# Performance work log

Measured on AMD Instinct MI355X. Metric: run time of the kernel, lower is better.

The kernel has to match this reference:

```python
import jax, jax.numpy as jnp
import numpy as np

B, C_IN, H, W = 4, 256, 48, 48
HEADS, HD = 8, 64
N = H * W
SCALE = 1.0 / (HD ** 0.5)


def setup_inputs() -> dict:
    key = jax.random.key(0)
    ks = jax.random.split(key, 5)
    x = jax.random.normal(ks[0], (B, C_IN, H, W), dtype=jnp.float32)
    # 1x1 conv weights, squeezed: [heads, head_channels, in_channels]
    Wq = jax.random.normal(ks[1], (HEADS, HD, C_IN), dtype=jnp.float32) * (C_IN ** -0.5)
    Wk = jax.random.normal(ks[2], (HEADS, HD, C_IN), dtype=jnp.float32) * (C_IN ** -0.5)
    Wv = jax.random.normal(ks[3], (HEADS, HD, C_IN), dtype=jnp.float32) * (C_IN ** -0.5)
    # output 1x1 conv: [in_channels, heads*head_channels]
    Wo = jax.random.normal(ks[4], (C_IN, HEADS * HD), dtype=jnp.float32) * ((HEADS * HD) ** -0.5)
    return {"x": x, "Wq": Wq, "Wk": Wk, "Wv": Wv, "Wo": Wo}


def reference(x, Wq, Wk, Wv, Wo):
    b, c, h, w = x.shape
    n = h * w
    xf = x.reshape(b, c, n)  # [B, C, N]
    # per-head 1x1 convs == batched projections -> [heads, B, N, HD]
    q = jnp.einsum('hdc,bcn->hbnd', Wq, xf)
    k = jnp.einsum('hdc,bcn->hbnd', Wk, xf)
    v = jnp.einsum('hdc,bcn->hbnd', Wv, xf)
    scores = jnp.einsum('hbnd,hbmd->hbnm', q, k) * SCALE  # [heads, B, N, N]
    probs = jax.nn.softmax(scores, axis=-1)
    ws = jnp.einsum('hbnm,hbmd->hbnd', probs, v)  # [heads, B, N, HD]
    # faithful replication of torch: transpose(1,2) then reshape(B, heads*HD, H, W)
    ws = jnp.transpose(ws, (0, 2, 1, 3))  # [heads, N, B, HD]
    ws = ws.reshape(b, HEADS * HD, h, w)
    out = jnp.einsum('oc,bchw->bohw', Wo, ws)  # output 1x1 conv
    return out
```

## Files before the change

kernel.cpp:

```cpp
#include <hip/hip_runtime.h>

#define B_     4
#define CIN    256
#define NTOK   2304
#define HEADS  8
#define HD     64
#define SCALE  0.125f
#define LOG2E  1.44269504088896f
#define QSCALE (SCALE * LOG2E)
#define PBIAS  4.0f
#define QKV_ELEMS (HEADS * B_ * NTOK * HD)
#define HBSTRIDE 147456
#define WSZ    131072

typedef _Float16 f16;
typedef _Float16 __attribute__((ext_vector_type(8))) h8v;
typedef _Float16 __attribute__((ext_vector_type(4))) h4v;
typedef ushort   __attribute__((ext_vector_type(8))) us8;
typedef float    __attribute__((ext_vector_type(16))) f16v;

__device__ inline uint pk2(float a, float b) {
    auto v = __builtin_amdgcn_cvt_pkrtz(a, b);
    return __builtin_bit_cast(uint, v);
}
#define EXP2(x) __builtin_amdgcn_exp2f(x)

#define GLOAD_LDS(g, l) __builtin_amdgcn_global_load_lds( \
    (const __attribute__((address_space(1))) unsigned int*)(g), \
    (__attribute__((address_space(3))) unsigned int*)(l), 16, 0, 0)

__global__ __launch_bounds__(256) void prep(
    const float* __restrict__ x,
    const float* __restrict__ Wq, const float* __restrict__ Wk,
    const float* __restrict__ Wv, const float* __restrict__ Wo,
    f16* __restrict__ wc, f16* __restrict__ woc, f16* __restrict__ xt)
{
    __shared__ float T[64][65];
    const int bid = blockIdx.x;
    const int tid = threadIdx.x;

    if (bid < 512) {
        int e4 = (bid * 256 + tid) * 4;
        const float* src; f16* dst; float mult = 1.0f; int off;
        if (e4 < WSZ)          { src = Wq; off = e4;           dst = wc;           mult = QSCALE; }
        else if (e4 < 2 * WSZ) { src = Wk; off = e4 - WSZ;     dst = wc + WSZ; }
        else if (e4 < 3 * WSZ) { src = Wv; off = e4 - 2 * WSZ; dst = wc + 2 * WSZ; }
        else                   { src = Wo; off = e4 - 3 * WSZ; dst = woc; }
        float4 r = *(const float4*)(src + off);
        h4v hv;
        hv.x = (f16)(r.x * mult); hv.y = (f16)(r.y * mult);
        hv.z = (f16)(r.z * mult); hv.w = (f16)(r.w * mult);
        *(h4v*)(dst + off) = hv;
        return;
    }

    const int r  = bid - 512;
    const int n0 = (r % 36) * 64;
    const int c0 = ((r / 36) % 4) * 64;
    const int b  = r / 144;
    const float* sb = x + ((size_t)b * CIN + c0) * NTOK;
    #pragma unroll
    for (int i = 0; i < 16; ++i) {
        int idx = tid + 256 * i;
        int rr = idx >> 6, ll = idx & 63;
        T[ll][rr] = sb[(size_t)rr * NTOK + n0 + ll];
    }
    __syncthreads();
    const size_t ob = ((size_t)b * NTOK + n0) * CIN + c0;
    #pragma unroll
    for (int i = 0; i < 4; ++i) {
        int idx = tid + 256 * i;
        int row = idx >> 4, c4 = (idx & 15) * 4;
        h4v v;
        v.x = (f16)T[row][c4 + 0]; v.y = (f16)T[row][c4 + 1];
        v.z = (f16)T[row][c4 + 2]; v.w = (f16)T[row][c4 + 3];
        *(h4v*)(xt + ob + (size_t)row * CIN + c4) = v;
    }
}

__global__ __launch_bounds__(128) void proj_mfma(
    const f16* __restrict__ wc, const f16* __restrict__ xt,
    f16* __restrict__ qh, f16* __restrict__ kh, f16* __restrict__ vth)
{
    const int ntile = blockIdx.x;
    const int hp    = blockIdx.y;
    const int b     = blockIdx.z;
    const int p     = hp >> 3, h = hp & 7;
    const int hb    = h * 4 + b;
    const f16* Wp = wc + ((size_t)p * 8 + h) * (HD * CIN);

    __shared__ __align__(16) f16 Ws[2][64][64], Xs[2][64][64];

    const int tid = threadIdx.x;
    const int w = tid >> 6, lane = tid & 63;
    const int lm = lane & 31, lh = lane >> 5;
    const int n_loc  = w * 32 + lm;
    const int n_glob = ntile * 64 + n_loc;

    const f16* xb = xt + ((size_t)b * NTOK + ntile * 64) * CIN;

    auto stage = [&](int buf, int c0) {
        const f16* src = (w == 0) ? Wp : xb;
        f16* dst = (w == 0) ? &Ws[buf][0][0] : &Xs[buf][0][0];
        #pragma unroll
        for (int i = 0; i < 8; ++i) {
            int g = i * 64 + lane; int row = g >> 3; int c = (g & 7) ^ (row & 7);
            GLOAD_LDS(src + (size_t)row * CIN + c0 + c * 8, dst + i * 512);
        }
    };

    f16v o0, o1;
    #pragma unroll
    for (int i = 0; i < 16; ++i) { o0[i] = 0.f; o1[i] = 0.f; }

    stage(0, 0);
    for (int c0 = 0; c0 < CIN; c0 += 64) {
        const int cur = (c0 >> 6) & 1;
        __syncthreads();
        if (c0 + 64 < CIN) stage(cur ^ 1, c0 + 64);
        #pragma unroll
        for (int s = 0; s < 4; ++s) {
            const int pp = ((2 * s + lh) ^ (lm & 7)) * 8;
            h8v a0 = *(const h8v*)&Ws[cur][lm][pp];
            h8v a1 = *(const h8v*)&Ws[cur][lm + 32][pp];
            h8v bh = *(const h8v*)&Xs[cur][n_loc][pp];
            o0 = __builtin_amdgcn_mfma_f32_32x32x16_f16(a0, bh, o0, 0, 0, 0);
            o1 = __builtin_amdgcn_mfma_f32_32x32x16_f16(a1, bh, o1, 0, 0, 0);
        }
    }

    const size_t hboff = (size_t)hb * HBSTRIDE;
    if (p < 2) {
        f16* oh = ((p == 0) ? qh : kh) + hboff + (size_t)n_glob * 64;
        #pragma unroll
        for (int t = 0; t < 2; ++t) {
            const f16v& oc = t ? o1 : o0;
            #pragma unroll
            for (int g = 0; g < 4; ++g) {
                int d0 = 8 * g + 4 * lh + 32 * t;
                h4v hv;
                hv.x = (f16)oc[4 * g + 0]; hv.y = (f16)oc[4 * g + 1];
                hv.z = (f16)oc[4 * g + 2]; hv.w = (f16)oc[4 * g + 3];
                *(h4v*)(oh + d0) = hv;
            }
        }
    } else {
        f16* oh = vth + hboff;
        #pragma unroll
        for (int t = 0; t < 2; ++t) {
            const f16v& oc = t ? o1 : o0;
            #pragma unroll
            for (int r = 0; r < 16; ++r) {
                int d = (r & 3) + 8 * (r >> 2) + 4 * lh + 32 * t;
                oh[(size_t)d * NTOK + n_glob] = (f16)oc[r];
            }
        }
    }
}

__global__ __launch_bounds__(256, 1) void attn_mfma(
    const f16* __restrict__ qh, const f16* __restrict__ kh,
    const f16* __restrict__ vth, f16* __restrict__ wsth)
{
    const int bid   = blockIdx.x;
    const int xcd   = bid & 7;
    const int slot  = bid >> 3;
    const int hb    = xcd * 4 + (slot / 18);
    const int rpair = slot % 18;
    const int h_    = hb >> 2, b = hb & 3;
    const int tid   = threadIdx.x;
    const int w     = tid >> 6;
    const int lane  = tid & 63;
    const int lm    = lane & 31;
    const int lh    = lane >> 5;
    const int qg    = w >> 1;
    const int ks    = w & 1;

    __shared__ __align__(16) f16 SMEM[2][2][2][64][64];

    const size_t hboff = (size_t)hb * HBSTRIDE;
    const int mA = rpair * 128 + qg * 64 + lm;
    const int mB = mA + 32;

    h8v QfA[4], QfB[4];
    #pragma unroll
    for (int s = 0; s < 4; ++s) {
        QfA[s] = *(const h8v*)(qh + hboff + (size_t)mA * 64 + (2 * s + lh) * 8);
        QfB[s] = *(const h8v*)(qh + hboff + (size_t)mB * 64 + (2 * s + lh) * 8);
    }

    f16v oA0, oA1, oB0, oB1;
    f16v sA0, sA1, sB0, sB1;
    #pragma unroll
    for (int i = 0; i < 16; ++i) { oA0[i] = 0.f; oA1[i] = 0.f; oB0[i] = 0.f; oB1[i] = 0.f; }
    float lsumA = 0.f, lsumB = 0.f;
    h8v pfA[4], pfB[4];

    const int  sv  = w >> 1;
    const int  stp = w & 1;
    const f16* gb  = (sv == 0) ? kh + hboff : vth + hboff;

    auto stage = [&](int tb, int ti) {
        const int kts = 2 * ti + stp;
        f16* dst = &SMEM[sv][tb][stp][0][0];
        #pragma unroll
        for (int i = 0; i < 8; ++i) {
            int g   = i * 64 + lane;
            int row = g >> 3;
            int c   = (g & 7) ^ (row & 7);
            const f16* src = (sv == 0)
                ? gb + kts * 4096 + row * 64 + c * 8
                : gb + (size_t)row * 2304 + kts * 64 + c * 8;
            GLOAD_LDS(src, dst + i * 512);
        }
    };

    auto DO_QK = [&](int tb) {
        #pragma unroll
        for (int i = 0; i < 16; ++i) {
            sA0[i] = -PBIAS; sA1[i] = -PBIAS; sB0[i] = -PBIAS; sB1[i] = -PBIAS;
        }
        #pragma unroll
        for (int s = 0; s < 4; ++s) {
            const int p = ((2 * s + lh) ^ (lm & 7)) * 8;
            h8v k0 = *(const h8v*)&SMEM[0][tb][ks][lm][p];
            h8v k1 = *(const h8v*)&SMEM[0][tb][ks][lm + 32][p];
            sA0 = __builtin_amdgcn_mfma_f32_32x32x16_f16(k0, QfA[s], sA0, 0, 0, 0);
            sA1 = __builtin_amdgcn_mfma_f32_32x32x16_f16(k1, QfA[s], sA1, 0, 0, 0);
            sB0 = __builtin_amdgcn_mfma_f32_32x32x16_f16(k0, QfB[s], sB0, 0, 0, 0);
            sB1 = __builtin_amdgcn_mfma_f32_32x32x16_f16(k1, QfB[s], sB1, 0, 0, 0);
        }
    };

    auto DO_SM = [&]() {
        float pa0 = 0.f, pa1 = 0.f, pa2 = 0.f, pa3 = 0.f;
        float pb0 = 0.f, pb1 = 0.f, pb2 = 0.f, pb3 = 0.f;
        #pragma unroll
        for (int i = 0; i < 16; i += 4) {
            sA0[i+0] = EXP2(sA0[i+0]); pa0 += sA0[i+0];
            sA0[i+1] = EXP2(sA0[i+1]); pa1 += sA0[i+1];
            sA0[i+2] = EXP2(sA0[i+2]); pa2 += sA0[i+2];
            sA0[i+3] = EXP2(sA0[i+3]); pa3 += sA0[i+3];
        }
        #pragma unroll
        for (int i = 0; i < 16; i += 4) {
            sA1[i+0] = EXP2(sA1[i+0]); pa0 += sA1[i+0];
            sA1[i+1] = EXP2(sA1[i+1]); pa1 += sA1[i+1];
            sA1[i+2] = EXP2(sA1[i+2]); pa2 += sA1[i+2];
            sA1[i+3] = EXP2(sA1[i+3]); pa3 += sA1[i+3];
        }
        #pragma unroll
        for (int i = 0; i < 16; i += 4) {
            sB0[i+0] = EXP2(sB0[i+0]); pb0 += sB0[i+0];
            sB0[i+1] = EXP2(sB0[i+1]); pb1 += sB0[i+1];
            sB0[i+2] = EXP2(sB0[i+2]); pb2 += sB0[i+2];
            sB0[i+3] = EXP2(sB0[i+3]); pb3 += sB0[i+3];
        }
        #pragma unroll
        for (int i = 0; i < 16; i += 4) {
            sB1[i+0] = EXP2(sB1[i+0]); pb0 += sB1[i+0];
            sB1[i+1] = EXP2(sB1[i+1]); pb1 += sB1[i+1];
            sB1[i+2] = EXP2(sB1[i+2]); pb2 += sB1[i+2];
            sB1[i+3] = EXP2(sB1[i+3]); pb3 += sB1[i+3];
        }
        lsumA += (pa0 + pa1) + (pa2 + pa3);
        lsumB += (pb0 + pb1) + (pb2 + pb3);

        #pragma unroll
        for (int s = 0; s < 4; ++s) {
            const int q2 = 8 * (s & 1);
            const f16v& ja = (s >> 1) ? sA1 : sA0;
            const f16v& jb = (s >> 1) ? sB1 : sB0;
            uint a0 = pk2(ja[q2 + 0], ja[q2 + 1]);
            uint a1 = pk2(ja[q2 + 2], ja[q2 + 3]);
            uint a2 = pk2(ja[q2 + 4], ja[q2 + 5]);
            uint a3 = pk2(ja[q2 + 6], ja[q2 + 7]);
            auto a02 = __builtin_amdgcn_permlane32_swap(a0, a2, false, false);
            auto a13 = __builtin_amdgcn_permlane32_swap(a1, a3, false, false);
            uint4 ua = { a02[0], a13[0], a02[1], a13[1] };
            pfA[s] = __builtin_bit_cast(h8v, ua);
            uint b0 = pk2(jb[q2 + 0], jb[q2 + 1]);
            uint b1 = pk2(jb[q2 + 2], jb[q2 + 3]);
            uint b2 = pk2(jb[q2 + 4], jb[q2 + 5]);
            uint b3 = pk2(jb[q2 + 6], jb[q2 + 7]);
            auto b02 = __builtin_amdgcn_permlane32_swap(b0, b2, false, false);
            auto b13 = __builtin_amdgcn_permlane32_swap(b1, b3, false, false);
            uint4 ub = { b02[0], b13[0], b02[1], b13[1] };
            pfB[s] = __builtin_bit_cast(h8v, ub);
        }
    };

    auto DO_PV = [&](int tb) {
        #pragma unroll
        for (int s = 0; s < 4; ++s) {
            const int p = ((2 * s + lh) ^ (lm & 7)) * 8;
            h8v v0 = *(const h8v*)&SMEM[1][tb][ks][lm][p];
            h8v v1 = *(const h8v*)&SMEM[1][tb][ks][lm + 32][p];
            oA0 = __builtin_amdgcn_mfma_f32_32x32x16_f16(v0, pfA[s], oA0, 0, 0, 0);
            oA1 = __builtin_amdgcn_mfma_f32_32x32x16_f16(v1, pfA[s], oA1, 0, 0, 0);
            oB0 = __builtin_amdgcn_mfma_f32_32x32x16_f16(v0, pfB[s], oB0, 0, 0, 0);
            oB1 = __builtin_amdgcn_mfma_f32_32x32x16_f16(v1, pfB[s], oB1, 0, 0, 0);
        }
    };

    if (sv == 0) stage(0, 0);
    __syncthreads();

    stage(sv == 0 ? 1 : 0, sv == 0 ? 1 : 0);
    __builtin_amdgcn_s_setprio(1);
    DO_QK(0);
    __builtin_amdgcn_s_setprio(0);
    __syncthreads();

    for (int t = 1; t < 18; ++t) {
        if (sv == 0) { if (t < 17) stage((t + 1) & 1, t + 1); }
        else         stage(t & 1, t);

        DO_SM();
        __builtin_amdgcn_s_setprio(1);
        DO_PV((t - 1) & 1);
        DO_QK(t & 1);
        __builtin_amdgcn_s_setprio(0);
        __syncthreads();
    }

    DO_SM();
    __builtin_amdgcn_s_setprio(1);
    DO_PV(1);
    __builtin_amdgcn_s_setprio(0);
    __syncthreads();

    float* red = (float*)&SMEM[0][0][0][0][0];
    if (ks == 1) {
        float* dA = red + (size_t)(qg * 128 + lane) * 33;
        float* dB = red + (size_t)(qg * 128 + 64 + lane) * 33;
        #pragma unroll
        for (int i = 0; i < 16; ++i) {
            dA[i] = oA0[i]; dA[16 + i] = oA1[i];
            dB[i] = oB0[i]; dB[16 + i] = oB1[i];
        }
        dA[32] = lsumA; dB[32] = lsumB;
    }
    __syncthreads();
    if (ks == 0) {
        const float* sA = red + (size_t)(qg * 128 + lane) * 33;
        const float* sB = red + (size_t)(qg * 128 + 64 + lane) * 33;
        #pragma unroll
        for (int i = 0; i < 16; ++i) {
            oA0[i] += sA[i]; oA1[i] += sA[16 + i];
            oB0[i] += sB[i]; oB1[i] += sB[16 + i];
        }
        lsumA += sA[32]; lsumB += sB[32];
        lsumA += __shfl_xor(lsumA, 32);
        lsumB += __shfl_xor(lsumB, 32);
        float invA = 1.0f / lsumA, invB = 1.0f / lsumB;

        f16* wrA = wsth + ((size_t)h_ * NTOK + mA) * 256 + b * 64;
        f16* wrB = wsth + ((size_t)h_ * NTOK + mB) * 256 + b * 64;
        #pragma unroll
        for (int g = 0; g < 4; ++g) {
            h4v r0, r1;
            r0.x = (f16)(oA0[4 * g + 0] * invA); r0.y = (f16)(oA0[4 * g + 1] * invA);
            r0.z = (f16)(oA0[4 * g + 2] * invA); r0.w = (f16)(oA0[4 * g + 3] * invA);
            *(h4v*)(wrA + 8 * g + 4 * lh) = r0;
            r1.x = (f16)(oA1[4 * g + 0] * invA); r1.y = (f16)(oA1[4 * g + 1] * invA);
            r1.z = (f16)(oA1[4 * g + 2] * invA); r1.w = (f16)(oA1[4 * g + 3] * invA);
            *(h4v*)(wrA + 32 + 8 * g + 4 * lh) = r1;
        }
        #pragma unroll
        for (int g = 0; g < 4; ++g) {
            h4v r0, r1;
            r0.x = (f16)(oB0[4 * g + 0] * invB); r0.y = (f16)(oB0[4 * g + 1] * invB);
            r0.z = (f16)(oB0[4 * g + 2] * invB); r0.w = (f16)(oB0[4 * g + 3] * invB);
            *(h4v*)(wrB + 8 * g + 4 * lh) = r0;
            r1.x = (f16)(oB1[4 * g + 0] * invB); r1.y = (f16)(oB1[4 * g + 1] * invB);
            r1.z = (f16)(oB1[4 * g + 2] * invB); r1.w = (f16)(oB1[4 * g + 3] * invB);
            *(h4v*)(wrB + 32 + 8 * g + 4 * lh) = r1;
        }
    }
}

__global__ __launch_bounds__(128) void outconv_mfma(
    const f16* __restrict__ woc, const f16* __restrict__ ws,
    float* __restrict__ out)
{
    const int ntile = blockIdx.x;
    const int otile = blockIdx.y;
    const int b     = blockIdx.z;

    __shared__ __align__(16) f16 Wos[2][64][64];
    __shared__ __align__(16) f16 Xs[2][64][72];

    const int tid = threadIdx.x;
    const int w = tid >> 6, lane = tid & 63;
    const int lm = lane & 31, lh = lane >> 5;
    const int n_loc  = w * 32 + lm;
    const int n_glob = ntile * 64 + n_loc;
    const int pr = tid >> 2;
    const int qn = tid & 3;

    const f16* Wb = woc + (size_t)(otile * 64) * 512;
    const f16* wsb = ws + (size_t)b * 512 * NTOK + ntile * 64 + qn * 16;

    auto stageW = [&](int buf, int c0) {
        #pragma unroll
        for (int j = 0; j < 4; ++j) {
            int i = w * 4 + j;
            int g = i * 64 + lane; int row = g >> 3; int c = (g & 7) ^ (row & 7);
            GLOAD_LDS(Wb + (size_t)row * 512 + c0 + c * 8,
                      &Wos[buf][0][0] + i * 512);
        }
    };

    uint4 x0, x1, x2, x3;
    auto loadB = [&](int c0) {
        const f16* r0 = wsb + (size_t)(c0 + 2 * pr) * NTOK;
        const f16* r1 = r0 + NTOK;
        x0 = *(const uint4*)(r0);
        x1 = *(const uint4*)(r0 + 8);
        x2 = *(const uint4*)(r1);
        x3 = *(const uint4*)(r1 + 8);
    };
    auto storeB = [&](int buf) {
        us8 a0 = __builtin_bit_cast(us8, x0), a1 = __builtin_bit_cast(us8, x1);
        us8 b0 = __builtin_bit_cast(us8, x2), b1 = __builtin_bit_cast(us8, x3);
        #pragma unroll
        for (int j = 0; j < 8; ++j) {
            *(uint*)&Xs[buf][qn * 16 + j][2 * pr]     = (uint)a0[j] | ((uint)b0[j] << 16);
            *(uint*)&Xs[buf][qn * 16 + 8 + j][2 * pr] = (uint)a1[j] | ((uint)b1[j] << 16);
        }
    };

    f16v o0, o1;
    #pragma unroll
    for (int i = 0; i < 16; ++i) { o0[i] = 0.f; o1[i] = 0.f; }

    stageW(0, 0);
    loadB(0);
    storeB(0);
    for (int c0 = 0; c0 < 512; c0 += 64) {
        const int cur = (c0 >> 6) & 1;
        __syncthreads();
        if (c0 + 64 < 512) { stageW(cur ^ 1, c0 + 64); loadB(c0 + 64); }
        #pragma unroll
        for (int s = 0; s < 4; ++s) {
            const int pp = ((2 * s + lh) ^ (lm & 7)) * 8;
            const int co = (2 * s + lh) * 8;
            h8v a0 = *(const h8v*)&Wos[cur][lm][pp];
            h8v a1 = *(const h8v*)&Wos[cur][lm + 32][pp];
            h8v bh = *(const h8v*)&Xs[cur][n_loc][co];
            o0 = __builtin_amdgcn_mfma_f32_32x32x16_f16(a0, bh, o0, 0, 0, 0);
            o1 = __builtin_amdgcn_mfma_f32_32x32x16_f16(a1, bh, o1, 0, 0, 0);
        }
        if (c0 + 64 < 512) storeB(cur ^ 1);
    }

    #pragma unroll
    for (int t = 0; t < 2; ++t) {
        const f16v& oc = t ? o1 : o0;
        #pragma unroll
        for (int r = 0; r < 16; ++r) {
            int orow = otile * 64 + (r & 3) + 8 * (r >> 2) + 4 * lh + 32 * t;
            out[((size_t)b * CIN + orow) * NTOK + n_glob] = oc[r];
        }
    }
}

extern "C" void kernel_launch(void* const* d_in, const int* in_sizes, int n_in,
                              void* d_out, int out_size, void* d_ws, size_t ws_size,
                              hipStream_t stream)
{
    const float* x  = (const float*)d_in[0];
    const float* Wq = (const float*)d_in[1];
    const float* Wk = (const float*)d_in[2];
    const float* Wv = (const float*)d_in[3];
    const float* Wo = (const float*)d_in[4];
    float* out = (float*)d_out;

    f16* qh   = (f16*)d_ws;
    f16* kh   = qh   + QKV_ELEMS;
    f16* vth  = kh   + QKV_ELEMS;
    f16* wsth = vth  + QKV_ELEMS;
    f16* xt   = wsth;
    f16* wc   = wsth + QKV_ELEMS;
    f16* woc  = wc   + 3 * WSZ;

    prep<<<dim3(1088), 256, 0, stream>>>(x, Wq, Wk, Wv, Wo, wc, woc, xt);
    proj_mfma<<<dim3(36, 24, 4), 128, 0, stream>>>(wc, xt, qh, kh, vth);
    attn_mfma<<<dim3(576), 256, 0, stream>>>(qh, kh, vth, wsth);
    outconv_mfma<<<dim3(36, 4, 4), 128, 0, stream>>>(woc, wsth, out);
}
```

Baseline: 193.6 us.

## Shrink attention blocks to two waves with per-wave self-staged K/V

The attention kernel moves from 256-thread blocks (two query groups with a key-split pair each) to 128-thread blocks covering 64 queries, launched as 1152 blocks with launch_bounds allowing three blocks per CU. Each wave now stages its own K and V tiles into a private LDS slice and synchronises with explicit vmcnt/lgkmcnt waits in place of block-wide __syncthreads in the main loop. The aim is to raise occupancy so waves overlap loads with MFMA work, and to drop barrier costs. In exchange it loses the double-buffered K/V prefetch and reads Q once per smaller tile. The hand-placed waitcnt counts must match the number of outstanding loads, or the kernel can read stale LDS data.

```diff
diff --git a/kernel.cpp b/kernel.cpp
--- a/kernel.cpp
+++ b/kernel.cpp
@@ -28,6 +28,11 @@
 #define GLOAD_LDS(g, l) __builtin_amdgcn_global_load_lds( \
     (const __attribute__((address_space(1))) unsigned int*)(g), \
     (__attribute__((address_space(3))) unsigned int*)(l), 16, 0, 0)
+
+#define VMFENCE(N) do { asm volatile("s_waitcnt vmcnt(" #N ")" ::: "memory"); \
+                        __builtin_amdgcn_sched_barrier(0); } while (0)
+#define LGKFENCE() do { asm volatile("s_waitcnt lgkmcnt(0)" ::: "memory"); \
+                        __builtin_amdgcn_sched_barrier(0); } while (0)
 
 __global__ __launch_bounds__(256) void prep(
     const float* __restrict__ x,
@@ -158,28 +163,26 @@
     }
 }
 
-__global__ __launch_bounds__(256, 1) void attn_mfma(
+__global__ __launch_bounds__(128, 3) void attn_mfma(
     const f16* __restrict__ qh, const f16* __restrict__ kh,
     const f16* __restrict__ vth, f16* __restrict__ wsth)
 {
     const int bid   = blockIdx.x;
     const int xcd   = bid & 7;
     const int slot  = bid >> 3;
-    const int hb    = xcd * 4 + (slot / 18);
-    const int rpair = slot % 18;
+    const int hb    = xcd * 4 + (slot / 36);
+    const int rtile = slot % 36;
     const int h_    = hb >> 2, b = hb & 3;
     const int tid   = threadIdx.x;
     const int w     = tid >> 6;
     const int lane  = tid & 63;
     const int lm    = lane & 31;
     const int lh    = lane >> 5;
-    const int qg    = w >> 1;
-    const int ks    = w & 1;
-
-    __shared__ __align__(16) f16 SMEM[2][2][2][64][64];
+
+    __shared__ __align__(16) f16 SMEM[2][2][64][64];
 
     const size_t hboff = (size_t)hb * HBSTRIDE;
-    const int mA = rpair * 128 + qg * 64 + lm;
+    const int mA = rtile * 64 + lm;
     const int mB = mA + 32;
 
     h8v QfA[4], QfB[4];
@@ -196,40 +199,45 @@
     float lsumA = 0.f, lsumB = 0.f;
     h8v pfA[4], pfB[4];
 
-    const int  sv  = w >> 1;
-    const int  stp = w & 1;
-    const f16* gb  = (sv == 0) ? kh + hboff : vth + hboff;
-
-    auto stage = [&](int tb, int ti) {
-        const int kts = 2 * ti + stp;
-        f16* dst = &SMEM[sv][tb][stp][0][0];
+    const f16* kb = kh + hboff;
+    const f16* vb = vth + hboff;
+
+    auto stageK = [&](int t) {
+        const int kts = 2 * t + w;
+        f16* dst = &SMEM[0][w][0][0];
         #pragma unroll
         for (int i = 0; i < 8; ++i) {
-            int g   = i * 64 + lane;
-            int row = g >> 3;
-            int c   = (g & 7) ^ (row & 7);
-            const f16* src = (sv == 0)
-                ? gb + kts * 4096 + row * 64 + c * 8
-                : gb + (size_t)row * 2304 + kts * 64 + c * 8;
-            GLOAD_LDS(src, dst + i * 512);
-        }
-    };
-
-    auto DO_QK = [&](int tb) {
+            int g = i * 64 + lane; int row = g >> 3; int c = (g & 7) ^ (row & 7);
+            GLOAD_LDS(kb + kts * 4096 + row * 64 + c * 8, dst + i * 512);
+        }
+    };
+    auto stageV = [&](int t) {
+        const int kts = 2 * t + w;
+        f16* dst = &SMEM[1][w][0][0];
+        #pragma unroll
+        for (int i = 0; i < 8; ++i) {
+            int g = i * 64 + lane; int row = g >> 3; int c = (g & 7) ^ (row & 7);
+            GLOAD_LDS(vb + (size_t)row * 2304 + kts * 64 + c * 8, dst + i * 512);
+        }
+    };
+
+    auto DO_QK = [&]() {
         #pragma unroll
         for (int i = 0; i < 16; ++i) {
             sA0[i] = -PBIAS; sA1[i] = -PBIAS; sB0[i] = -PBIAS; sB1[i] = -PBIAS;
         }
+        __builtin_amdgcn_s_setprio(1);
         #pragma unroll
         for (int s = 0; s < 4; ++s) {
             const int p = ((2 * s + lh) ^ (lm & 7)) * 8;
-            h8v k0 = *(const h8v*)&SMEM[0][tb][ks][lm][p];
-            h8v k1 = *(const h8v*)&SMEM[0][tb][ks][lm + 32][p];
+            h8v k0 = *(const h8v*)&SMEM[0][w][lm][p];
+            h8v k1 = *(const h8v*)&SMEM[0][w][lm + 32][p];
             sA0 = __builtin_amdgcn_mfma_f32_32x32x16_f16(k0, QfA[s], sA0, 0, 0, 0);
             sA1 = __builtin_amdgcn_mfma_f32_32x32x16_f16(k1, QfA[s], sA1, 0, 0, 0);
             sB0 = __builtin_amdgcn_mfma_f32_32x32x16_f16(k0, QfB[s], sB0, 0, 0, 0);
             sB1 = __builtin_amdgcn_mfma_f32_32x32x16_f16(k1, QfB[s], sB1, 0, 0, 0);
         }
+        __builtin_amdgcn_s_setprio(0);
     };
 
     auto DO_SM = [&]() {
@@ -290,67 +298,65 @@
         }
     };
 
-    auto DO_PV = [&](int tb) {
+    auto DO_PV = [&]() {
+        __builtin_amdgcn_s_setprio(1);
         #pragma unroll
         for (int s = 0; s < 4; ++s) {
             const int p = ((2 * s + lh) ^ (lm & 7)) * 8;
-            h8v v0 = *(const h8v*)&SMEM[1][tb][ks][lm][p];
-            h8v v1 = *(const h8v*)&SMEM[1][tb][ks][lm + 32][p];
+            h8v v0 = *(const h8v*)&SMEM[1][w][lm][p];
+            h8v v1 = *(const h8v*)&SMEM[1][w][lm + 32][p];
             oA0 = __builtin_amdgcn_mfma_f32_32x32x16_f16(v0, pfA[s], oA0, 0, 0, 0);
             oA1 = __builtin_amdgcn_mfma_f32_32x32x16_f16(v1, pfA[s], oA1, 0, 0, 0);
             oB0 = __builtin_amdgcn_mfma_f32_32x32x16_f16(v0, pfB[s], oB0, 0, 0, 0);
             oB1 = __builtin_amdgcn_mfma_f32_32x32x16_f16(v1, pfB[s], oB1, 0, 0, 0);
         }
-    };
-
-    if (sv == 0) stage(0, 0);
+        __builtin_amdgcn_s_setprio(0);
+    };
+
+    stageK(0);
+    stageV(0);
+    VMFENCE(0);
+
+    for (int t = 0; t < 17; ++t) {
+        VMFENCE(8);
+        DO_QK();
+        LGKFENCE();
+        stageK(t + 1);
+        DO_SM();
+        VMFENCE(8);
+        DO_PV();
+        LGKFENCE();
+        stageV(t + 1);
+    }
+    VMFENCE(8);
+    DO_QK();
+    DO_SM();
+    VMFENCE(0);
+    DO_PV();
+
     __syncthreads();
-
-    stage(sv == 0 ? 1 : 0, sv == 0 ? 1 : 0);
-    __builtin_amdgcn_s_setprio(1);
-    DO_QK(0);
-    __builtin_amdgcn_s_setprio(0);
+    float* red  = (float*)&SMEM[0][0][0][0];
+    float* lred = red + 64 * 65;
+    if (w == 1) {
+        float* d = red + (size_t)lane * 65;
+        #pragma unroll
+        for (int i = 0; i < 16; ++i) {
+            d[i]      = oA0[i]; d[16 + i] = oA1[i];
+            d[32 + i] = oB0[i]; d[48 + i] = oB1[i];
+        }
+        lred[2 * lane]     = lsumA;
+        lred[2 * lane + 1] = lsumB;
+    }
     __syncthreads();
-
-    for (int t = 1; t < 18; ++t) {
-        if (sv == 0) { if (t < 17) stage((t + 1) & 1, t + 1); }
-        else         stage(t & 1, t);
-
-        DO_SM();
-        __builtin_amdgcn_s_setprio(1);
-        DO_PV((t - 1) & 1);
-        DO_QK(t & 1);
-        __builtin_amdgcn_s_setprio(0);
-        __syncthreads();
-    }
-
-    DO_SM();
-    __builtin_amdgcn_s_setprio(1);
-    DO_PV(1);
-    __builtin_amdgcn_s_setprio(0);
-    __syncthreads();
-
-    float* red = (float*)&SMEM[0][0][0][0][0];
-    if (ks == 1) {
-        float* dA = red + (size_t)(qg * 128 + lane) * 33;
-        float* dB = red + (size_t)(qg * 128 + 64 + lane) * 33;
+    if (w == 0) {
+        const float* sp = red + (size_t)lane * 65;
         #pragma unroll
         for (int i = 0; i < 16; ++i) {
-            dA[i] = oA0[i]; dA[16 + i] = oA1[i];
-            dB[i] = oB0[i]; dB[16 + i] = oB1[i];
-        }
-        dA[32] = lsumA; dB[32] = lsumB;
-    }
-    __syncthreads();
-    if (ks == 0) {
-        const float* sA = red + (size_t)(qg * 128 + lane) * 33;
-        const float* sB = red + (size_t)(qg * 128 + 64 + lane) * 33;
-        #pragma unroll
-        for (int i = 0; i < 16; ++i) {
-            oA0[i] += sA[i]; oA1[i] += sA[16 + i];
-            oB0[i] += sB[i]; oB1[i] += sB[16 + i];
-        }
-        lsumA += sA[32]; lsumB += sB[32];
+            oA0[i] += sp[i];      oA1[i] += sp[16 + i];
+            oB0[i] += sp[32 + i]; oB1[i] += sp[48 + i];
+        }
+        lsumA += lred[2 * lane];
+        lsumB += lred[2 * lane + 1];
         lsumA += __shfl_xor(lsumA, 32);
         lsumB += __shfl_xor(lsumB, 32);
         float invA = 1.0f / lsumA, invB = 1.0f / lsumB;
@@ -487,6 +493,6 @@
 
     prep<<<dim3(1088), 256, 0, stream>>>(x, Wq, Wk, Wv, Wo, wc, woc, xt);
     proj_mfma<<<dim3(36, 24, 4), 128, 0, stream>>>(wc, xt, qh, kh, vth);
-    attn_mfma<<<dim3(576), 256, 0, stream>>>(qh, kh, vth, wsth);
+    attn_mfma<<<dim3(1152), 128, 0, stream>>>(qh, kh, vth, wsth);
     outconv_mfma<<<dim3(36, 4, 4), 128, 0, stream>>>(woc, wsth, out);
 }
```

New measurement: 324.3 us. 67.5% more time.
